# Kernel optimization log

Hardware: AMD Instinct MI355X
Metric: run time of the kernel (lower is better)

## Reference

```python
import jax, jax.numpy as jnp
import numpy as np

WEIGHT_ENERGY = 0.1
WEIGHT_COV = 0.005
EPS = 1e-9
COV_EPS = 1e-6
TWO_PI = 2.0 * np.pi


def setup_inputs() -> dict:
    key = jax.random.key(0)
    k1, k2 = jax.random.split(key)
    z = jax.random.normal(k1, (16, 256, 64, 32), dtype=jnp.float32)
    gamma = jax.random.uniform(k2, (16, 256, 64, 8), dtype=jnp.float32)
    return {"z": z, "gamma": gamma}


def _gmm_loss(z, gamma):
    # z: [B,T,F,D], gamma: [B,T,F,K]
    D = z.shape[-1]
    N = z.shape[0] * z.shape[1] * z.shape[2]
    sum_gamma = jnp.sum(gamma, axis=(0, 1, 2))            # [K]
    phi = sum_gamma / N                                    # [K]
    mu = jnp.einsum('btfk,btfd->kd', gamma, z) / sum_gamma[:, None]  # [K,D]
    z_mu = z[..., None, :] - mu                            # [B,T,F,K,D]
    # covariance per component (gamma-weighted outer products)
    cov = jnp.einsum('btfk,btfkd,btfke->kde', gamma, z_mu, z_mu) / sum_gamma[:, None, None]
    eye = jnp.eye(D, dtype=z.dtype)
    cov = cov + CO_EPS_I(eye)
    cov_k = cov + EPS * eye                                # [K,D,D]
    cov_inv = jnp.linalg.inv(cov_k)                        # [K,D,D]
    L = jnp.linalg.cholesky(cov_k * TWO_PI)                # [K,D,D]
    det_cov = jnp.prod(jnp.diagonal(L, axis1=-2, axis2=-1), axis=-1)  # [K] (= sqrt(det(2pi*cov)))
    cov_diag = jnp.sum(1.0 / jnp.diagonal(cov_k, axis1=-2, axis2=-1))
    # quadratic-form energy, fused reduction over D
    E_z = -0.5 * jnp.einsum('btfkd,kde,btfke->btfk', z_mu, cov_inv, z_mu)
    E_z = jnp.exp(E_z)
    E_z = -jnp.log(jnp.sum(phi * E_z / jnp.sqrt(det_cov), axis=-1) + COV_EPS)
    sample_energy = jnp.mean(E_z)
    sample_energy = jnp.where(jnp.isfinite(sample_energy), sample_energy, 0.0)
    cov_diag = jnp.where(jnp.isfinite(cov_diag), cov_diag, 0.0)
    return WEIGHT_ENERGY * sample_energy + WEIGHT_COV * cov_diag


def CO_EPS_I(eye):
    return COV_EPS * eye


def reference(z, gamma):
    return _gmm_loss(z, gamma)
```

## Files before the change

### kernel.cpp

```cpp
#include <hip/hip_runtime.h>
#include <hip/hip_bf16.h>
#include <math.h>

#define NS (16*256*64)
#define D 32
#define K 8

typedef __attribute__((ext_vector_type(8))) short bf16x8;
typedef __attribute__((ext_vector_type(8))) float f32x8;
typedef __attribute__((ext_vector_type(8))) __bf16 bf16v8;
typedef __attribute__((ext_vector_type(16))) float f32x16;

#define WS_ENERGY   0
#define WS_COVDIAG  1
#define WS_DONE     2
#define WS_C        16
#define WS_COEF     24
#define WS_SG       32
#define WS_S1       64
#define WS_S2       1024
#define WS_FRAGA    9216
#define WS_FRAGB    13312
#define WS_PART     16384
#define PART_STRIDE 8456

__device__ __forceinline__ bf16x8 cvt8(f32x8 v) {
    union { bf16v8 h; bf16x8 s; } u;
    u.h = __builtin_convertvector(v, bf16v8);
    return u.s;
}
__device__ __forceinline__ short f2bf1(float f) {
    union { __bf16 h; short s; } u;
    u.h = (__bf16)f;
    return u.s;
}
__device__ __forceinline__ float rdlane(float v, int lane) {
    return __uint_as_float(__builtin_amdgcn_readlane(__float_as_uint(v), lane));
}

__global__ __launch_bounds__(256) void k_moments(const float* __restrict__ z,
                                                 const float* __restrict__ g,
                                                 float* __restrict__ part) {
    __shared__ float zs[64][32];
    __shared__ float gs[64][8];
    const int t   = threadIdx.x;
    const int w   = t >> 6;
    const int l   = t & 63;
    const int col = l & 31;
    const int nh  = l >> 5;
    const int k0  = 2 * w;

    f32x16 acc0 = {}, acc1 = {};
    float s1a = 0.f, s1b = 0.f, sga = 0.f, sgb = 0.f;

    for (int c = blockIdx.x; c < NS / 64; c += gridDim.x) {
        const int base = c * 64;
        __syncthreads();
        const float4* zsrc = (const float4*)(z + (size_t)base * 32);
        float4* zdst = (float4*)(&zs[0][0]);
        zdst[t]       = zsrc[t];
        zdst[t + 256] = zsrc[t + 256];
        if (t < 128) {
            ((float4*)(&gs[0][0]))[t] = ((const float4*)(g + (size_t)base * 8))[t];
        }
        __syncthreads();
#pragma unroll
        for (int sc = 0; sc < 4; sc++) {
            const int s0 = sc * 16 + nh * 8;
            f32x8 zv, p0, p1;
#pragma unroll
            for (int j = 0; j < 8; j++) {
                float zf = zs[s0 + j][col];
                float2 gg = *(const float2*)(&gs[s0 + j][k0]);
                zv[j] = zf;
                p0[j] = gg.x * zf;
                p1[j] = gg.y * zf;
                s1a += p0[j];  s1b += p1[j];
                sga += gg.x;   sgb += gg.y;
            }
            bf16x8 af = cvt8(zv), b0 = cvt8(p0), b1 = cvt8(p1);
            acc0 = __builtin_amdgcn_mfma_f32_32x32x16_bf16(af, b0, acc0, 0, 0, 0);
            acc1 = __builtin_amdgcn_mfma_f32_32x32x16_bf16(af, b1, acc1, 0, 0, 0);
        }
    }
    s1a += __shfl_xor(s1a, 32);  s1b += __shfl_xor(s1b, 32);
    sga += __shfl_xor(sga, 32);  sgb += __shfl_xor(sgb, 32);

    float* pb = part + (size_t)blockIdx.x * PART_STRIDE;
#pragma unroll
    for (int r = 0; r < 16; r++) {
        int row = (r & 3) + 8 * (r >> 2) + 4 * nh;
        pb[(size_t)k0 * 1024 + row * 32 + col]       = acc0[r];
        pb[(size_t)(k0 + 1) * 1024 + row * 32 + col] = acc1[r];
    }
    if (l < 32) {
        pb[8192 + k0 * 32 + col]       = s1a;
        pb[8192 + (k0 + 1) * 32 + col] = s1b;
    }
    if (l == 0) { pb[8448 + k0] = sga; pb[8448 + k0 + 1] = sgb; }
}

__global__ __launch_bounds__(1024) void k_reduce(float* __restrict__ ws, int nblk) {
    __shared__ float red[16][64];
    const int t  = threadIdx.x;
    const int el = t & 63;
    const int bg = t >> 6;
    const int e  = blockIdx.x * 64 + el;
    const float* part = ws + WS_PART;
    float s = 0.0f;
    if (e < PART_STRIDE) {
        for (int b = bg; b < nblk; b += 16)
            s += part[(size_t)b * PART_STRIDE + e];
    }
    red[bg][el] = s;
    __syncthreads();
#pragma unroll
    for (int h = 8; h > 0; h >>= 1) {
        if (bg < h) red[bg][el] += red[bg + h][el];
        __syncthreads();
    }
    if (bg == 0 && e < PART_STRIDE) {
        float v = red[0][el];
        if (e < 8192)       ws[WS_S2 + e] = v;
        else if (e < 8448)  ws[WS_S1 + (e - 8192)] = v;
        else                ws[WS_SG + (e - 8448)] = v;
    }
    if (blockIdx.x == 0) {
        if (t < 512) ws[WS_FRAGB + t] = 0.0f;
        if (t == 0) {
            ws[WS_ENERGY] = 0.0f;
            ws[WS_COVDIAG] = 0.0f;
            ((unsigned*)ws)[WS_DONE] = 0u;
        }
    }
}

__global__ __launch_bounds__(64) void k_prep(float* __restrict__ ws) {
    __shared__ float Am[32][33];
    __shared__ float mus[32];
    __shared__ float bLs[32];

    const int k   = blockIdx.x;
    const int l   = threadIdx.x;
    const int c32 = l & 31;
    const bool right = l >= 32;

    const float sgk = ws[WS_SG + k];
    if (l < 32) mus[l] = ws[WS_S1 + k * 32 + l] / sgk;
    __syncthreads();
    const float mc  = mus[c32];
    const float rsg = 1.0f / sgk;

    float x[32];
    float dval = 1.0f;
#pragma unroll
    for (int r = 0; r < 32; r++) {
        float v;
        if (right) {
            v = (r == c32) ? 1.0f : 0.0f;
        } else {
            v = ws[WS_S2 + k * 1024 + r * 32 + c32] * rsg - mus[r] * mc;
            if (r == c32) { v += 1.0e-6f + 1.0e-9f; dval = v; }
        }
        x[r] = v;
    }

    {
        float tdi = right ? 0.0f : 1.0f / dval;
#pragma unroll
        for (int m = 1; m < 64; m <<= 1) tdi += __shfl_xor(tdi, m);
        if (l == 0) atomicAdd(&ws[WS_COVDIAG], tdi);
    }

    float logdet = 0.0f;
#pragma unroll
    for (int j = 0; j < 32; j++) {
        float piv = rdlane(x[j], j);
        float rp  = 1.0f / piv;
        logdet += __logf(piv);
        x[j] *= rp;
#pragma unroll
        for (int r = 0; r < 32; r++) {
            if (r == j) continue;
            float m = rdlane(x[r], j);
            x[r] -= m * x[j];
        }
    }
    if (right) {
#pragma unroll
        for (int r = 0; r < 32; r++) Am[r][c32] = x[r];
    }
    __syncthreads();

    if (l == 0) {
        float phi = sgk / (float)NS;
        ws[WS_COEF + k] = phi * __expf(-(8.0f * 1.8378770664093453f + 0.25f * logdet));
    }

    if (l < 32) {
        float s = 0.0f;
#pragma unroll
        for (int c = 0; c < 32; c++) s += Am[c32][c] * mus[c];
        bLs[c32] = s;
    }
    __syncthreads();
    {
        float cm = (l < 32) ? mus[c32] * bLs[c32] : 0.0f;
#pragma unroll
        for (int m = 1; m < 64; m <<= 1) cm += __shfl_xor(cm, m);
        if (l == 0) ws[WS_C + k] = cm;
    }

    {
        const int ph = l >> 5;
#pragma unroll
        for (int h = 0; h < 2; h++) {
            int r = c32, cb = ph * 8 + 16 * h;
            unsigned uu[4];
#pragma unroll
            for (int q = 0; q < 4; q++) {
                unsigned lo2 = (unsigned short)f2bf1(Am[r][cb + 2 * q]);
                unsigned hi2 = (unsigned short)f2bf1(Am[r][cb + 2 * q + 1]);
                uu[q] = lo2 | (hi2 << 16);
            }
            ((uint4*)(ws + WS_FRAGA))[(k * 2 + h) * 64 + l] = make_uint4(uu[0], uu[1], uu[2], uu[3]);
        }
        if (c32 == k) {
#pragma unroll
            for (int h = 0; h < 2; h++) {
                int cb = ph * 8 + 16 * h;
                unsigned uu[4];
#pragma unroll
                for (int q = 0; q < 4; q++) {
                    unsigned lo2 = (unsigned short)f2bf1(bLs[cb + 2 * q]);
                    unsigned hi2 = (unsigned short)f2bf1(bLs[cb + 2 * q + 1]);
                    uu[q] = lo2 | (hi2 << 16);
                }
                ((uint4*)(ws + WS_FRAGB))[h * 64 + l] = make_uint4(uu[0], uu[1], uu[2], uu[3]);
            }
        }
    }
}

__global__ __launch_bounds__(512) void k_energy(const float* __restrict__ z,
                                                float* __restrict__ ws,
                                                float* __restrict__ out) {
    __shared__ uint4 frg[1152];
    __shared__ float redw[8];
    const int t   = threadIdx.x;
    const int w   = t >> 6;
    const int l   = t & 63;
    const int col = l & 31;
    const int nh  = l >> 5;

    for (int i = t; i < 1152; i += 512) frg[i] = ((const uint4*)(ws + WS_FRAGA))[i];
    float cf[8], cc[8];
#pragma unroll
    for (int k = 0; k < 8; k++) { cf[k] = ws[WS_COEF + k]; cc[k] = ws[WS_C + k]; }
    __syncthreads();

    float En = 0.0f;
    for (int ci = 0; ci < 2; ci++) {
        const int chunk = (blockIdx.x * 8 + w) * 2 + ci;
        const int n0 = chunk * 32;
        const float* zb = z + (size_t)(n0 + col) * 32 + nh * 8;
        float4 a0 = *(const float4*)(zb + 0);
        float4 a1 = *(const float4*)(zb + 4);
        float4 a2 = *(const float4*)(zb + 16);
        float4 a3 = *(const float4*)(zb + 20);
        f32x8 zlo = {a0.x,a0.y,a0.z,a0.w,a1.x,a1.y,a1.z,a1.w};
        f32x8 zhi = {a2.x,a2.y,a2.z,a2.w,a3.x,a3.y,a3.z,a3.w};
        bf16x8 b0 = cvt8(zlo), b1 = cvt8(zhi);
        float olo[4], ohi[4];
#pragma unroll
        for (int j = 0; j < 4; j++) {
            float mlo = nh ? zlo[j] : zlo[j + 4];
            float mhi = nh ? zhi[j] : zhi[j + 4];
            olo[j] = __shfl_xor(mlo, 32);
            ohi[j] = __shfl_xor(mhi, 32);
        }
        float zdot[16];
#pragma unroll
        for (int j = 0; j < 4; j++) {
            zdot[j]      = nh ? olo[j]     : zlo[j];
            zdot[4 + j]  = nh ? zlo[4 + j] : olo[j];
            zdot[8 + j]  = nh ? ohi[j]     : zhi[j];
            zdot[12 + j] = nh ? zhi[4 + j] : ohi[j];
        }
        f32x16 acc2 = {};
        {
            bf16x8 fb0 = *(const bf16x8*)&frg[1024 + l];
            bf16x8 fb1 = *(const bf16x8*)&frg[1024 + 64 + l];
            acc2 = __builtin_amdgcn_mfma_f32_32x32x16_bf16(fb0, b0, acc2, 0, 0, 0);
            acc2 = __builtin_amdgcn_mfma_f32_32x32x16_bf16(fb1, b1, acc2, 0, 0, 0);
        }
        float oth[4];
#pragma unroll
        for (int r = 0; r < 4; r++) oth[r] = __shfl_xor(acc2[r], 32);
        float pk[8];
#pragma unroll
        for (int k = 0; k < 8; k++) {
            bf16x8 fa0 = *(const bf16x8*)&frg[(k * 2 + 0) * 64 + l];
            bf16x8 fa1 = *(const bf16x8*)&frg[(k * 2 + 1) * 64 + l];
            f32x16 acc = {};
            acc = __builtin_amdgcn_mfma_f32_32x32x16_bf16(fa0, b0, acc, 0, 0, 0);
            acc = __builtin_amdgcn_mfma_f32_32x32x16_bf16(fa1, b1, acc, 0, 0, 0);
            float p = 0.0f;
#pragma unroll
            for (int r = 0; r < 16; r++) p += acc[r] * zdot[r];
            p += __shfl_xor(p, 32);
            pk[k] = p;
        }
        float ssum = 0.0f;
#pragma unroll
        for (int k = 0; k < 8; k++) {
            float d2 = (k < 4) ? (nh ? oth[k] : acc2[k]) : (nh ? acc2[k - 4] : oth[k - 4]);
            float E = pk[k] - 2.0f * d2 + cc[k];
            ssum += cf[k] * __expf(-0.5f * E);
        }
        En += -__logf(ssum + 1.0e-6f);
    }
#pragma unroll
    for (int m = 1; m < 64; m <<= 1) En += __shfl_xor(En, m);
    if (l == 0) redw[w] = En;
    __syncthreads();
    if (t == 0) {
        float s = 0.0f;
#pragma unroll
        for (int i = 0; i < 8; i++) s += redw[i];
        atomicAdd(&ws[WS_ENERGY], s);
        __threadfence();
        unsigned old = atomicAdd((unsigned*)ws + WS_DONE, 1u);
        if (old == gridDim.x - 1) {
            float se = atomicAdd(&ws[WS_ENERGY], 0.0f);
            se = se * 0.5f / (float)NS;
            if (!isfinite(se)) se = 0.0f;
            float cd = ws[WS_COVDIAG];
            if (!isfinite(cd)) cd = 0.0f;
            out[0] = 0.1f * se + 0.005f * cd;
        }
    }
}

extern "C" void kernel_launch(void* const* d_in, const int* in_sizes, int n_in,
                              void* d_out, int out_size, void* d_ws, size_t ws_size,
                              hipStream_t stream) {
    const float* z = (const float*)d_in[0];
    const float* g = (const float*)d_in[1];
    float* out = (float*)d_out;
    float* ws  = (float*)d_ws;

    long avail = (long)(ws_size / 4) - WS_PART;
    int nblk = (int)(avail / PART_STRIDE);
    if (nblk > 512) nblk = 512;
    if (nblk < 1)   nblk = 1;

    k_moments<<<nblk, 256, 0, stream>>>(z, g, ws + WS_PART);
    k_reduce<<<(PART_STRIDE + 63) / 64, 1024, 0, stream>>>(ws, nblk);
    k_prep<<<8, 64, 0, stream>>>(ws);
    k_energy<<<512, 512, 0, stream>>>(z, ws, out);
}
```

Measured before the change: 77.92 us.

## Prefetch next moments chunk into registers, stage bf16 transposed tiles, drop energy LDS staging

The moments kernel now loads the next chunk of z and gamma into registers while the current chunk is processed. It stores them to shared memory as transposed bf16 tiles with an XOR swizzle, so the MFMA operand can be read as a single vector load instead of eight scalar reads. The energy kernel stops copying the precomputed fragments into shared memory with a barrier and reads them straight from global memory (cached), keeping the B fragments in registers. This trades more register pressure and repeated global fragment loads for less load latency and fewer barriers. The gamma-weighted products are now formed from bf16-rounded inputs, which slightly changes numerics.

```diff
diff --git a/kernel.cpp b/kernel.cpp
--- a/kernel.cpp
+++ b/kernel.cpp
@@ -3,6 +3,7 @@
 #include <math.h>
 
 #define NS (16*256*64)
+#define NCHUNK (NS/64)
 #define D 32
 #define K 8
 
@@ -29,10 +30,15 @@
     u.h = __builtin_convertvector(v, bf16v8);
     return u.s;
 }
-__device__ __forceinline__ short f2bf1(float f) {
-    union { __bf16 h; short s; } u;
+__device__ __forceinline__ unsigned short f2bf1(float f) {
+    union { __bf16 h; unsigned short s; } u;
     u.h = (__bf16)f;
     return u.s;
+}
+__device__ __forceinline__ float bf2f(unsigned short u) {
+    union { unsigned u32; float f; } v;
+    v.u32 = ((unsigned)u) << 16;
+    return v.f;
 }
 __device__ __forceinline__ float rdlane(float v, int lane) {
     return __uint_as_float(__builtin_amdgcn_readlane(__float_as_uint(v), lane));
@@ -41,46 +47,82 @@
 __global__ __launch_bounds__(256) void k_moments(const float* __restrict__ z,
                                                  const float* __restrict__ g,
                                                  float* __restrict__ part) {
-    __shared__ float zs[64][32];
-    __shared__ float gs[64][8];
+    __shared__ __align__(16) unsigned short zbt[32][72];
+    __shared__ __align__(16) unsigned short gbt[8][72];
     const int t   = threadIdx.x;
     const int w   = t >> 6;
     const int l   = t & 63;
     const int col = l & 31;
     const int nh  = l >> 5;
     const int k0  = 2 * w;
+    const int sz  = t >> 2;
+    const int dq  = (t & 3) * 8;
 
     f32x16 acc0 = {}, acc1 = {};
     float s1a = 0.f, s1b = 0.f, sga = 0.f, sgb = 0.f;
 
-    for (int c = blockIdx.x; c < NS / 64; c += gridDim.x) {
-        const int base = c * 64;
+    int c = blockIdx.x;
+    float4 za, zb4, ga4, gb4;
+    {
+        const float* zp = z + ((size_t)(c * 64 + sz)) * 32 + dq;
+        za  = *(const float4*)zp;
+        zb4 = *(const float4*)(zp + 4);
+        if (t < 64) {
+            const float* gp = g + ((size_t)(c * 64 + t)) * 8;
+            ga4 = *(const float4*)gp;
+            gb4 = *(const float4*)(gp + 4);
+        }
+    }
+
+    for (; c < NCHUNK; c += gridDim.x) {
         __syncthreads();
-        const float4* zsrc = (const float4*)(z + (size_t)base * 32);
-        float4* zdst = (float4*)(&zs[0][0]);
-        zdst[t]       = zsrc[t];
-        zdst[t + 256] = zsrc[t + 256];
-        if (t < 128) {
-            ((float4*)(&gs[0][0]))[t] = ((const float4*)(g + (size_t)base * 8))[t];
+        {
+            float zf8[8] = {za.x, za.y, za.z, za.w, zb4.x, zb4.y, zb4.z, zb4.w};
+#pragma unroll
+            for (int i = 0; i < 8; i++) {
+                int d = dq + i;
+                zbt[d][sz ^ (((d >> 3) & 3) << 3)] = f2bf1(zf8[i]);
+            }
+            if (t < 64) {
+                float gf8[8] = {ga4.x, ga4.y, ga4.z, ga4.w, gb4.x, gb4.y, gb4.z, gb4.w};
+#pragma unroll
+                for (int k = 0; k < 8; k++) gbt[k][t] = f2bf1(gf8[k]);
+            }
+        }
+        {
+            int cn = c + gridDim.x;
+            if (cn < NCHUNK) {
+                const float* zp = z + ((size_t)(cn * 64 + sz)) * 32 + dq;
+                za  = *(const float4*)zp;
+                zb4 = *(const float4*)(zp + 4);
+                if (t < 64) {
+                    const float* gp = g + ((size_t)(cn * 64 + t)) * 8;
+                    ga4 = *(const float4*)gp;
+                    gb4 = *(const float4*)(gp + 4);
+                }
+            }
         }
         __syncthreads();
+        const int xs = ((col >> 3) & 3) << 3;
 #pragma unroll
         for (int sc = 0; sc < 4; sc++) {
             const int s0 = sc * 16 + nh * 8;
-            f32x8 zv, p0, p1;
+            bf16x8 af = *(const bf16x8*)&zbt[col][s0 ^ xs];
+            bf16x8 g0 = *(const bf16x8*)&gbt[k0][s0];
+            bf16x8 g1 = *(const bf16x8*)&gbt[k0 + 1][s0];
+            f32x8 p0, p1;
 #pragma unroll
             for (int j = 0; j < 8; j++) {
-                float zf = zs[s0 + j][col];
-                float2 gg = *(const float2*)(&gs[s0 + j][k0]);
-                zv[j] = zf;
-                p0[j] = gg.x * zf;
-                p1[j] = gg.y * zf;
+                float zf = bf2f((unsigned short)af[j]);
+                float ga = bf2f((unsigned short)g0[j]);
+                float gb = bf2f((unsigned short)g1[j]);
+                p0[j] = ga * zf;
+                p1[j] = gb * zf;
                 s1a += p0[j];  s1b += p1[j];
-                sga += gg.x;   sgb += gg.y;
-            }
-            bf16x8 af = cvt8(zv), b0 = cvt8(p0), b1 = cvt8(p1);
-            acc0 = __builtin_amdgcn_mfma_f32_32x32x16_bf16(af, b0, acc0, 0, 0, 0);
-            acc1 = __builtin_amdgcn_mfma_f32_32x32x16_bf16(af, b1, acc1, 0, 0, 0);
+                sga += ga;     sgb += gb;
+            }
+            acc0 = __builtin_amdgcn_mfma_f32_32x32x16_bf16(af, cvt8(p0), acc0, 0, 0, 0);
+            acc1 = __builtin_amdgcn_mfma_f32_32x32x16_bf16(af, cvt8(p1), acc1, 0, 0, 0);
         }
     }
     s1a += __shfl_xor(s1a, 32);  s1b += __shfl_xor(s1b, 32);
@@ -219,8 +261,8 @@
             unsigned uu[4];
 #pragma unroll
             for (int q = 0; q < 4; q++) {
-                unsigned lo2 = (unsigned short)f2bf1(Am[r][cb + 2 * q]);
-                unsigned hi2 = (unsigned short)f2bf1(Am[r][cb + 2 * q + 1]);
+                unsigned lo2 = f2bf1(Am[r][cb + 2 * q]);
+                unsigned hi2 = f2bf1(Am[r][cb + 2 * q + 1]);
                 uu[q] = lo2 | (hi2 << 16);
             }
             ((uint4*)(ws + WS_FRAGA))[(k * 2 + h) * 64 + l] = make_uint4(uu[0], uu[1], uu[2], uu[3]);
@@ -232,8 +274,8 @@
                 unsigned uu[4];
 #pragma unroll
                 for (int q = 0; q < 4; q++) {
-                    unsigned lo2 = (unsigned short)f2bf1(bLs[cb + 2 * q]);
-                    unsigned hi2 = (unsigned short)f2bf1(bLs[cb + 2 * q + 1]);
+                    unsigned lo2 = f2bf1(bLs[cb + 2 * q]);
+                    unsigned hi2 = f2bf1(bLs[cb + 2 * q + 1]);
                     uu[q] = lo2 | (hi2 << 16);
                 }
                 ((uint4*)(ws + WS_FRAGB))[h * 64 + l] = make_uint4(uu[0], uu[1], uu[2], uu[3]);
@@ -245,7 +287,6 @@
 __global__ __launch_bounds__(512) void k_energy(const float* __restrict__ z,
                                                 float* __restrict__ ws,
                                                 float* __restrict__ out) {
-    __shared__ uint4 frg[1152];
     __shared__ float redw[8];
     const int t   = threadIdx.x;
     const int w   = t >> 6;
@@ -253,11 +294,13 @@
     const int col = l & 31;
     const int nh  = l >> 5;
 
-    for (int i = t; i < 1152; i += 512) frg[i] = ((const uint4*)(ws + WS_FRAGA))[i];
+    const uint4* fragA = (const uint4*)(ws + WS_FRAGA);
+    const uint4* fragB = (const uint4*)(ws + WS_FRAGB);
     float cf[8], cc[8];
 #pragma unroll
     for (int k = 0; k < 8; k++) { cf[k] = ws[WS_COEF + k]; cc[k] = ws[WS_C + k]; }
-    __syncthreads();
+    uint4 fbu0 = fragB[l];
+    uint4 fbu1 = fragB[64 + l];
 
     float En = 0.0f;
     for (int ci = 0; ci < 2; ci++) {
@@ -288,23 +331,19 @@
             zdot[12 + j] = nh ? zhi[4 + j] : ohi[j];
         }
         f32x16 acc2 = {};
-        {
-            bf16x8 fb0 = *(const bf16x8*)&frg[1024 + l];
-            bf16x8 fb1 = *(const bf16x8*)&frg[1024 + 64 + l];
-            acc2 = __builtin_amdgcn_mfma_f32_32x32x16_bf16(fb0, b0, acc2, 0, 0, 0);
-            acc2 = __builtin_amdgcn_mfma_f32_32x32x16_bf16(fb1, b1, acc2, 0, 0, 0);
-        }
+        acc2 = __builtin_amdgcn_mfma_f32_32x32x16_bf16(*(const bf16x8*)&fbu0, b0, acc2, 0, 0, 0);
+        acc2 = __builtin_amdgcn_mfma_f32_32x32x16_bf16(*(const bf16x8*)&fbu1, b1, acc2, 0, 0, 0);
         float oth[4];
 #pragma unroll
         for (int r = 0; r < 4; r++) oth[r] = __shfl_xor(acc2[r], 32);
         float pk[8];
 #pragma unroll
         for (int k = 0; k < 8; k++) {
-            bf16x8 fa0 = *(const bf16x8*)&frg[(k * 2 + 0) * 64 + l];
-            bf16x8 fa1 = *(const bf16x8*)&frg[(k * 2 + 1) * 64 + l];
+            uint4 fa0u = fragA[(k * 2 + 0) * 64 + l];
+            uint4 fa1u = fragA[(k * 2 + 1) * 64 + l];
             f32x16 acc = {};
-            acc = __builtin_amdgcn_mfma_f32_32x32x16_bf16(fa0, b0, acc, 0, 0, 0);
-            acc = __builtin_amdgcn_mfma_f32_32x32x16_bf16(fa1, b1, acc, 0, 0, 0);
+            acc = __builtin_amdgcn_mfma_f32_32x32x16_bf16(*(const bf16x8*)&fa0u, b0, acc, 0, 0, 0);
+            acc = __builtin_amdgcn_mfma_f32_32x32x16_bf16(*(const bf16x8*)&fa1u, b1, acc, 0, 0, 0);
             float p = 0.0f;
 #pragma unroll
             for (int r = 0; r < 16; r++) p += acc[r] * zdot[r];
```

New measurement: 79.48 us. 2.0% more time.
